# Kernel tuning notes

Measured on AMD Instinct MI355X. Metric: run time of the kernel, lower is better.

The kernel has to match this reference:

```python
import jax, jax.numpy as jnp
import numpy as np

E, C, H, W = 64, 8, 32, 32  # E zonotope rows (1 center + 63 error terms)


def setup_inputs() -> dict:
    key = jax.random.key(0)
    x = jax.random.normal(key, (E, C, H, W), dtype=jnp.float32)
    # Zero center => lower < 0 < upper everywhere, so every element crosses
    # and the number of new error terms equals C*H*W (fixed output shape).
    x = x.at[0].set(0.0)
    return {"x": x}


def reference(x):
    e = x.shape[0]
    content_shape = x.shape[1:]
    n = int(np.prod(content_shape))  # max possible new error terms

    err = jnp.sum(jnp.abs(x[1:]), axis=0)
    upper = x[0] + err
    lower = x[0] - err

    cross = (lower * upper < 0).astype(x.dtype)   # crossing-zero mask
    nonneg = (lower >= 0).astype(x.dtype)         # strictly positive mask

    lam = nonneg + cross * upper / (upper - lower)
    lam = jnp.where(jnp.isnan(lam), 0.5, lam)
    # torch assigns lambda via .data (detached from the autograd graph)
    lam = jax.lax.stop_gradient(lam)

    delta = jnp.maximum(-lam * lower, (1.0 - lam) * upper)

    head = (delta / 2 + lam * x[0]) * cross + x[0] * nonneg          # new center
    body = x[1:] * (lam * cross + nonneg)                            # scaled old error terms

    # Vectorized stream-compaction scatter replacing the scripted .item() loop:
    # element k (flat order) with cross==True goes to tail row cumsum(cross)[k]-1.
    flat_cond = cross.reshape(-1) > 0
    vals = (delta / 2).reshape(-1)
    rows = jnp.cumsum(flat_cond.astype(jnp.int32)) - 1
    rows = jnp.clip(rows, 0, n - 1)
    tail = jnp.zeros((n, n), dtype=x.dtype)
    # (row, col) pairs are unique per column; masked-out elements write 0 (no-op).
    tail = tail.at[rows, jnp.arange(n)].set(jnp.where(flat_cond, vals, 0.0))

    return jnp.concatenate(
        [head[None], body, tail.reshape((n,) + content_shape)], axis=0
    )
```

## Files before the change

### kernel.cpp

```cpp
#include <hip/hip_runtime.h>
#include <math.h>

#define EROWS 64
#define NCOL  8192
#define TAIL_OFF (EROWS * NCOL)
#define TAIL_F4 (NCOL * NCOL / 4)
#define ROW_F4  (NCOL / 4)

#define WS_VAL(ws)     ((float*)(ws))
#define WS_FLAG(ws)    ((int*)((char*)(ws) + 32768))
#define WS_COLOF(ws)   ((int*)((char*)(ws) + 65536))
#define WS_TAILVAL(ws) ((float*)((char*)(ws) + 98304))
#define WS_COUNT(ws)   ((int*)((char*)(ws) + 131072))

__global__ void headbody_kernel(const float* __restrict__ x,
                                float* __restrict__ out,
                                float* __restrict__ val,
                                int* __restrict__ flag) {
    int k = blockIdx.x * blockDim.x + threadIdx.x;
    if (k >= NCOL) return;

    float err = 0.f;
    for (int e = 1; e < EROWS; ++e)
        err += fabsf(x[e * NCOL + k]);

    float x0    = x[k];
    float upper = x0 + err;
    float lower = x0 - err;

    float cross  = (lower * upper < 0.f) ? 1.f : 0.f;
    float nonneg = (lower >= 0.f) ? 1.f : 0.f;

    float lam = nonneg + cross * upper / (upper - lower);
    if (isnan(lam)) lam = 0.5f;

    float delta = fmaxf(-lam * lower, (1.f - lam) * upper);

    out[k] = (delta * 0.5f + lam * x0) * cross + x0 * nonneg;

    float scale = lam * cross + nonneg;
    val[k]  = delta * 0.5f;
    flag[k] = (cross > 0.f) ? 1 : 0;

    for (int e = 1; e < EROWS; ++e)
        out[e * NCOL + k] = x[e * NCOL + k] * scale;
}

__global__ void scan_kernel(const float* __restrict__ val,
                            const int* __restrict__ flag,
                            int* __restrict__ colof,
                            float* __restrict__ tailval,
                            int* __restrict__ count) {
    const int t = threadIdx.x;
    const int PER = NCOL / 1024;

    int f[PER];
    int s = 0;
    for (int j = 0; j < PER; ++j) {
        f[j] = flag[t * PER + j];
        s += f[j];
    }

    __shared__ int sh[1024];
    sh[t] = s;
    __syncthreads();

    for (int off = 1; off < 1024; off <<= 1) {
        int v = (t >= off) ? sh[t - off] : 0;
        __syncthreads();
        sh[t] += v;
        __syncthreads();
    }
    int running = (t == 0) ? 0 : sh[t - 1];

    for (int j = 0; j < PER; ++j) {
        int k = t * PER + j;
        if (f[j]) {
            colof[running]   = k;
            tailval[running] = val[k];
            ++running;
        }
    }
    if (t == 1023) *count = sh[1023];
}

__global__ void tail_kernel(const int* __restrict__ colof,
                            const float* __restrict__ tailval,
                            const int* __restrict__ count,
                            float* __restrict__ out) {
    int q  = blockIdx.x * blockDim.x + threadIdx.x;
    int r  = q >> 11;
    int c0 = (q & 2047) << 2;

    int cnt = *count;
    int   col = (r < cnt) ? colof[r]   : -1;
    float tv  = (r < cnt) ? tailval[r] : 0.f;

    float4 v;
    v.x = (col == c0 + 0) ? tv : 0.f;
    v.y = (col == c0 + 1) ? tv : 0.f;
    v.z = (col == c0 + 2) ? tv : 0.f;
    v.w = (col == c0 + 3) ? tv : 0.f;

    ((float4*)out)[TAIL_OFF / 4 + q] = v;
}

extern "C" void kernel_launch(void* const* d_in, const int* in_sizes, int n_in,
                              void* d_out, int out_size, void* d_ws, size_t ws_size,
                              hipStream_t stream) {
    const float* x = (const float*)d_in[0];
    float* out = (float*)d_out;

    headbody_kernel<<<NCOL / 256, 256, 0, stream>>>(x, out, WS_VAL(d_ws), WS_FLAG(d_ws));
    scan_kernel<<<1, 1024, 0, stream>>>(WS_VAL(d_ws), WS_FLAG(d_ws),
                                        WS_COLOF(d_ws), WS_TAILVAL(d_ws), WS_COUNT(d_ws));
    tail_kernel<<<TAIL_F4 / 256, 256, 0, stream>>>(WS_COLOF(d_ws), WS_TAILVAL(d_ws),
                                                   WS_COUNT(d_ws), out);
}
```

Baseline: 271.9 us.

## Move body scaling into fused vectorized write kernel with nontemporal tail stores

The column-stats kernel now only computes per-column lambda/scale and stores the scale to workspace. The body rescaling moves into a combined write kernel that also emits the tail, which is now one block per row with nontemporal float4 stores. The scan drops from 1024 threads with a shared-memory Hillis-Steele scan to 256 threads using wave shuffles and vector loads. This is meant to cut the 256MB tail write cost, improve body write coalescing and shorten the serial scan. In exchange x is read twice.

```diff
diff --git a/kernel.cpp b/kernel.cpp
--- a/kernel.cpp
+++ b/kernel.cpp
@@ -4,19 +4,26 @@
 #define EROWS 64
 #define NCOL  8192
 #define TAIL_OFF (EROWS * NCOL)
-#define TAIL_F4 (NCOL * NCOL / 4)
 #define ROW_F4  (NCOL / 4)
+#define BODY_F4 ((EROWS - 1) * ROW_F4)
+#define BODY_BLOCKS (BODY_F4 / 256)
+#define TAIL_BLOCKS NCOL
+
+typedef float vf4 __attribute__((ext_vector_type(4)));
+typedef int   vi4 __attribute__((ext_vector_type(4)));
 
 #define WS_VAL(ws)     ((float*)(ws))
 #define WS_FLAG(ws)    ((int*)((char*)(ws) + 32768))
 #define WS_COLOF(ws)   ((int*)((char*)(ws) + 65536))
 #define WS_TAILVAL(ws) ((float*)((char*)(ws) + 98304))
 #define WS_COUNT(ws)   ((int*)((char*)(ws) + 131072))
+#define WS_SCALE(ws)   ((float*)((char*)(ws) + 135168))
 
-__global__ void headbody_kernel(const float* __restrict__ x,
+__global__ void colstats_kernel(const float* __restrict__ x,
                                 float* __restrict__ out,
                                 float* __restrict__ val,
-                                int* __restrict__ flag) {
+                                int* __restrict__ flag,
+                                float* __restrict__ scale) {
     int k = blockIdx.x * blockDim.x + threadIdx.x;
     if (k >= NCOL) return;
 
@@ -36,14 +43,10 @@
 
     float delta = fmaxf(-lam * lower, (1.f - lam) * upper);
 
-    out[k] = (delta * 0.5f + lam * x0) * cross + x0 * nonneg;
-
-    float scale = lam * cross + nonneg;
-    val[k]  = delta * 0.5f;
-    flag[k] = (cross > 0.f) ? 1 : 0;
-
-    for (int e = 1; e < EROWS; ++e)
-        out[e * NCOL + k] = x[e * NCOL + k] * scale;
+    out[k]   = (delta * 0.5f + lam * x0) * cross + x0 * nonneg;
+    val[k]   = delta * 0.5f;
+    flag[k]  = (cross > 0.f) ? 1 : 0;
+    scale[k] = lam * cross + nonneg;
 }
 
 __global__ void scan_kernel(const float* __restrict__ val,
@@ -51,27 +54,33 @@
                             int* __restrict__ colof,
                             float* __restrict__ tailval,
                             int* __restrict__ count) {
-    const int t = threadIdx.x;
-    const int PER = NCOL / 1024;
+    const int t    = threadIdx.x;
+    const int lane = t & 63;
+    const int wave = t >> 6;
+    const int PER  = NCOL / 256;
 
     int f[PER];
-    int s = 0;
-    for (int j = 0; j < PER; ++j) {
-        f[j] = flag[t * PER + j];
-        s += f[j];
+    int mysum = 0;
+    const vi4* fp = (const vi4*)(flag + t * PER);
+    for (int j = 0; j < PER / 4; ++j) {
+        vi4 v = fp[j];
+        f[4*j+0] = v.x; f[4*j+1] = v.y; f[4*j+2] = v.z; f[4*j+3] = v.w;
+        mysum += v.x + v.y + v.z + v.w;
     }
 
-    __shared__ int sh[1024];
-    sh[t] = s;
+    int s = mysum;
+    for (int off = 1; off < 64; off <<= 1) {
+        int v = __shfl_up(s, off);
+        if (lane >= off) s += v;
+    }
+
+    __shared__ int wsum[4];
+    if (lane == 63) wsum[wave] = s;
     __syncthreads();
+    int wbase = 0;
+    for (int w = 0; w < wave; ++w) wbase += wsum[w];
 
-    for (int off = 1; off < 1024; off <<= 1) {
-        int v = (t >= off) ? sh[t - off] : 0;
-        __syncthreads();
-        sh[t] += v;
-        __syncthreads();
-    }
-    int running = (t == 0) ? 0 : sh[t - 1];
+    int running = wbase + s - mysum;
 
     for (int j = 0; j < PER; ++j) {
         int k = t * PER + j;
@@ -81,28 +90,43 @@
             ++running;
         }
     }
-    if (t == 1023) *count = sh[1023];
+    if (t == 255) *count = wsum[0] + wsum[1] + wsum[2] + wsum[3];
 }
 
-__global__ void tail_kernel(const int* __restrict__ colof,
-                            const float* __restrict__ tailval,
-                            const int* __restrict__ count,
-                            float* __restrict__ out) {
-    int q  = blockIdx.x * blockDim.x + threadIdx.x;
-    int r  = q >> 11;
-    int c0 = (q & 2047) << 2;
+__global__ void write_kernel(const float* __restrict__ x,
+                             const float* __restrict__ scale,
+                             const int* __restrict__ colof,
+                             const float* __restrict__ tailval,
+                             const int* __restrict__ count,
+                             float* __restrict__ out) {
+    const int tid = threadIdx.x;
 
-    int cnt = *count;
-    int   col = (r < cnt) ? colof[r]   : -1;
-    float tv  = (r < cnt) ? tailval[r] : 0.f;
+    if (blockIdx.x < BODY_BLOCKS) {
+        int b = blockIdx.x * 256 + tid;
+        int j = b & (ROW_F4 - 1);
+        int e = 1 + (b >> 11);
+        vf4 xv = ((const vf4*)x)[e * ROW_F4 + j];
+        vf4 sv = ((const vf4*)scale)[j];
+        ((vf4*)out)[e * ROW_F4 + j] = xv * sv;
+    } else {
+        int r   = blockIdx.x - BODY_BLOCKS;
+        int cnt = *count;
+        int   col = (r < cnt) ? colof[r]   : -1;
+        float tv  = (r < cnt) ? tailval[r] : 0.f;
 
-    float4 v;
-    v.x = (col == c0 + 0) ? tv : 0.f;
-    v.y = (col == c0 + 1) ? tv : 0.f;
-    v.z = (col == c0 + 2) ? tv : 0.f;
-    v.w = (col == c0 + 3) ? tv : 0.f;
-
-    ((float4*)out)[TAIL_OFF / 4 + q] = v;
+        vf4* rowp = (vf4*)out + (TAIL_OFF / 4) + (size_t)r * ROW_F4;
+        #pragma unroll
+        for (int i = 0; i < ROW_F4 / 256; ++i) {
+            int j  = i * 256 + tid;
+            int c0 = j << 2;
+            vf4 v;
+            v.x = (col == c0 + 0) ? tv : 0.f;
+            v.y = (col == c0 + 1) ? tv : 0.f;
+            v.z = (col == c0 + 2) ? tv : 0.f;
+            v.w = (col == c0 + 3) ? tv : 0.f;
+            __builtin_nontemporal_store(v, rowp + j);
+        }
+    }
 }
 
 extern "C" void kernel_launch(void* const* d_in, const int* in_sizes, int n_in,
@@ -111,9 +135,10 @@
     const float* x = (const float*)d_in[0];
     float* out = (float*)d_out;
 
-    headbody_kernel<<<NCOL / 256, 256, 0, stream>>>(x, out, WS_VAL(d_ws), WS_FLAG(d_ws));
-    scan_kernel<<<1, 1024, 0, stream>>>(WS_VAL(d_ws), WS_FLAG(d_ws),
-                                        WS_COLOF(d_ws), WS_TAILVAL(d_ws), WS_COUNT(d_ws));
-    tail_kernel<<<TAIL_F4 / 256, 256, 0, stream>>>(WS_COLOF(d_ws), WS_TAILVAL(d_ws),
-                                                   WS_COUNT(d_ws), out);
+    colstats_kernel<<<NCOL / 256, 256, 0, stream>>>(x, out, WS_VAL(d_ws),
+                                                    WS_FLAG(d_ws), WS_SCALE(d_ws));
+    scan_kernel<<<1, 256, 0, stream>>>(WS_VAL(d_ws), WS_FLAG(d_ws),
+                                       WS_COLOF(d_ws), WS_TAILVAL(d_ws), WS_COUNT(d_ws));
+    write_kernel<<<BODY_BLOCKS + TAIL_BLOCKS, 256, 0, stream>>>(
+        x, WS_SCALE(d_ws), WS_COLOF(d_ws), WS_TAILVAL(d_ws), WS_COUNT(d_ws), out);
 }
```

Result: slower. 291.2 us (+7.1%).
